# Performance work log

Hardware: AMD Instinct MI355X
Metric: run time of the kernel (lower is better)

The kernel has to match this reference:

```python
import jax, jax.numpy as jnp
import numpy as np

N = 20000
NNBR = 64
MESH = (64, 64, 64)
ORDER = 4          # B-spline interpolation order
ALPHA = 0.35       # Ewald splitting parameter (1/Angstrom)
BOX = 73.68        # cubic box edge (Angstrom)
KE = 14.399645478425668  # Coulomb constant, eV*Angstrom/e^2


def _Mn(x, n):
    """Cardinal B-spline M_n(x), support [0, n]."""
    if n == 2:
        return jnp.maximum(0.0, 1.0 - jnp.abs(x - 1.0))
    return (x * _Mn(x, n - 1) + (n - x) * _Mn(x - 1.0, n - 1)) / (n - 1)


def _bspline_fac(K):
    """|b(m)|^-2 ... i.e. 1/|Euler spline denominator|^2 per mesh dim."""
    m = jnp.arange(K, dtype=jnp.float32)
    k = jnp.arange(ORDER - 1, dtype=jnp.float32)
    Mv = _Mn(k + 1.0, ORDER)                       # M_n(1..n-1)
    phase = 2.0 * jnp.pi * m[:, None] * k[None, :] / K
    dre = jnp.sum(Mv * jnp.cos(phase), axis=1)
    dim = jnp.sum(Mv * jnp.sin(phase), axis=1)
    return 1.0 / (dre * dre + dim * dim)


def _pme_energy(positions, charges, cell, nbr, shifts):
    n = positions.shape[0]
    # ---------------- real-space short-range sum ----------------
    i_idx = jnp.arange(n)[:, None]
    valid = (nbr >= 0) & ~((nbr == i_idx) & jnp.all(shifts == 0, axis=-1))
    j = jnp.where(nbr >= 0, nbr, 0)
    rvec = positions[j] + shifts.astype(positions.dtype) @ cell - positions[:, None, :]
    r2 = jnp.sum(rvec * rvec, axis=-1)
    r = jnp.sqrt(jnp.where(valid, r2, 1.0))
    qq = charges[:, None] * charges[j]
    e_real = 0.5 * jnp.sum(jnp.where(valid, qq * jax.scipy.special.erfc(ALPHA * r) / r, 0.0))
    # ---------------- B-spline charge spreading ----------------
    Kx, Ky, Kz = MESH
    frac = positions @ jnp.linalg.inv(cell)        # cell rows = lattice vectors
    u = frac * jnp.array(MESH, dtype=positions.dtype)
    base = jnp.floor(u)
    t = u - base                                   # in [0, 1)
    basei = base.astype(jnp.int32)
    offs = jnp.arange(ORDER)
    wx = _Mn(t[:, 0:1] + offs, ORDER)              # [N, ORDER]
    wy = _Mn(t[:, 1:2] + offs, ORDER)
    wz = _Mn(t[:, 2:3] + offs, ORDER)
    ix = (basei[:, 0:1] - offs) % Kx
    iy = (basei[:, 1:2] - offs) % Ky
    iz = (basei[:, 2:3] - offs) % Kz
    W = (charges[:, None] * wx)[:, :, None, None] * wy[:, None, :, None] * wz[:, None, None, :]
    IDX = (ix[:, :, None, None] * Ky + iy[:, None, :, None]) * Kz + iz[:, None, None, :]
    mesh = jnp.zeros(Kx * Ky * Kz, positions.dtype).at[IDX.reshape(-1)].add(W.reshape(-1)).reshape(MESH)
    # ---------------- reciprocal-space FFT convolution ----------------
    Q = jnp.fft.fftn(mesh)
    Brec = 2.0 * jnp.pi * jnp.linalg.inv(cell).T   # rows are reciprocal vectors
    mx = (jnp.fft.fftfreq(Kx) * Kx).astype(positions.dtype)
    my = (jnp.fft.fftfreq(Ky) * Ky).astype(positions.dtype)
    mz = (jnp.fft.fftfreq(Kz) * Kz).astype(positions.dtype)
    kvec = (mx[:, None, None, None] * Brec[0] + my[None, :, None, None] * Brec[1]
            + mz[None, None, :, None] * Brec[2])
    k2 = jnp.sum(kvec * kvec, axis=-1)
    a2 = ALPHA * ALPHA
    kern = jnp.where(k2 > 0, jnp.exp(-k2 / (4.0 * a2)) / jnp.where(k2 > 0, k2, 1.0), 0.0)
    C = _bspline_fac(Kx)[:, None, None] * _bspline_fac(Ky)[None, :, None] * _bspline_fac(Kz)[None, None, :]
    vol = jnp.abs(jnp.linalg.det(cell))
    e_rec = (2.0 * jnp.pi / vol) * jnp.sum(kern * C * (Q.real ** 2 + Q.imag ** 2))
    # ---------------- self + neutralizing background ----------------
    qtot = jnp.sum(charges)
    e_self = -(ALPHA / jnp.sqrt(jnp.pi)) * jnp.sum(charges * charges)
    e_bg = -(jnp.pi / (2.0 * a2 * vol)) * qtot * qtot
    return e_real + e_rec + e_self + e_bg


def setup_inputs() -> dict:
    key = jax.random.key(0)
    k1, k2, k3 = jax.random.split(key, 3)
    positions = jax.random.uniform(k1, (N, 3), jnp.float32) * BOX
    q = jax.random.normal(k2, (N,), jnp.float32)
    q = q - jnp.mean(q)  # neutral system
    cell = BOX * jnp.eye(3, dtype=jnp.float32)
    nbr = jax.random.randint(k3, (N, NNBR), 0, N, jnp.int32)
    shifts = jnp.zeros((N, NNBR, 3), jnp.int32)
    return {"positions": positions, "node_charges": q, "cell": cell,
            "neighbor_matrix": nbr, "neighbor_shifts": shifts}


def reference(positions, node_charges, cell, neighbor_matrix, neighbor_shifts):
    def e_strain(pos, q, c, eps):
        F = jnp.eye(3, dtype=pos.dtype) + eps
        return _pme_energy(pos @ F, q, c @ F, neighbor_matrix, neighbor_shifts)

    eps0 = jnp.zeros((3, 3), positions.dtype)
    e, (g_pos, g_eps) = jax.value_and_grad(e_strain, argnums=(0, 3))(
        positions, node_charges, cell, eps0)
    vol = jnp.abs(jnp.linalg.det(cell))
    energies = e.reshape(1) * KE
    forces = -g_pos * KE
    virial = -0.5 * (g_eps + g_eps.T) * KE
    stresses = (virial / vol)[None]
    return energies, forces, stresses
```

## Files before the change

kernel.cpp:

```cpp
#include <hip/hip_runtime.h>
#include <math.h>

#define NATOM 20000
#define NNBR  64
#define KM    64
#define KM3   (KM*KM*KM)
#define NPAIR (NATOM*NNBR)

#define ALPHA_C 0.35f
#define KE_C    14.399645478425668f
#define TWO_OVER_SQRTPI 1.1283791670955126f
#define TWOPI_F 6.2831853071795864f
#define PI_F    3.14159265358979f
#define RC2     661.2244898f

#define WS_RE    0
#define WS_IM    (KM3)
#define WS_MESH  (2*KM3)
#define WS_GJ    (3*KM3)
#define WS_PART  (3*KM3 + 3*NATOM)
#define WS_FI    (WS_PART + 1024)
#define WS_POSQ  (WS_FI + 3*NATOM)
#define WS_NBS   (WS_POSQ + 4*NATOM)
#define ZERO_LEN (KM3 + 3*NATOM + 1024)

__device__ __forceinline__ float M2f(float x){ return fmaxf(0.f, 1.f - fabsf(x - 1.f)); }
__device__ __forceinline__ float M3f(float x){ return (x*M2f(x) + (3.f-x)*M2f(x-1.f)) * 0.5f; }
__device__ __forceinline__ float M4f(float x){ return (x*M3f(x) + (4.f-x)*M3f(x-1.f)) * (1.f/3.f); }

__device__ __forceinline__ float wsum64(float v){
#pragma unroll
  for(int off=32; off>0; off>>=1) v += __shfl_xor(v, off, 64);
  return v;
}

__device__ __forceinline__ float hinv9(const float* __restrict__ cell, float* h){
  float m00=cell[0],m01=cell[1],m02=cell[2];
  float m10=cell[3],m11=cell[4],m12=cell[5];
  float m20=cell[6],m21=cell[7],m22=cell[8];
  float det = m00*(m11*m22-m12*m21) - m01*(m10*m22-m12*m20) + m02*(m10*m21-m11*m20);
  float id = 1.f/det;
  h[0]=(m11*m22-m12*m21)*id; h[1]=(m02*m21-m01*m22)*id; h[2]=(m01*m12-m02*m11)*id;
  h[3]=(m12*m20-m10*m22)*id; h[4]=(m00*m22-m02*m20)*id; h[5]=(m02*m10-m00*m12)*id;
  h[6]=(m10*m21-m11*m20)*id; h[7]=(m01*m20-m00*m21)*id; h[8]=(m00*m11-m01*m10)*id;
  return fabsf(det);
}

__device__ __forceinline__ void fill_tw(int t, float* twr, float* twi){
  if(t < 64){
    float ss, cc; sincosf((TWOPI_F/64.f)*(float)t, &ss, &cc);
    twr[t] = cc; twi[t] = -ss;
  }
}

__device__ __forceinline__ void fft64t(float& xr, float& xi, int lane,
                                       const float* __restrict__ twr,
                                       const float* __restrict__ twi, float sgn){
#pragma unroll
  for(int k=0;k<6;k++){
    int half = 32 >> k;
    float or_ = __shfl_xor(xr, half, 64);
    float oi_ = __shfl_xor(xi, half, 64);
    bool hi = (lane & half) != 0;
    float sr = hi ? (or_ - xr) : (xr + or_);
    float si = hi ? (oi_ - xi) : (xi + oi_);
    int e = (lane & (half-1)) << k;
    float wr2 = hi ? twr[e] : 1.f;
    float wi2 = hi ? sgn*twi[e] : 0.f;
    xr = sr*wr2 - si*wi2;
    xi = sr*wi2 + si*wr2;
  }
  int rev = __brev((unsigned)lane) >> 26;
  xr = __shfl(xr, rev, 64);
  xi = __shfl(xi, rev, 64);
}

__global__ __launch_bounds__(256) void init_kernel(
    const float* __restrict__ pos, const float* __restrict__ q,
    const int* __restrict__ nbr, const int* __restrict__ shifts,
    float* __restrict__ zbase, float4* __restrict__ posq, int* __restrict__ nbs){
  int t = blockIdx.x*256 + threadIdx.x;
  if(t < ZERO_LEN) zbase[t] = 0.f;
  if(t < NATOM)
    posq[t] = make_float4(pos[3*t], pos[3*t+1], pos[3*t+2], q[t]);
  if(t < NPAIR){
    int j = nbr[t];
    int sx=shifts[3*t], sy=shifts[3*t+1], sz=shifts[3*t+2];
    int v;
    if(j < 0) v = -1;
    else v = (j & 0x7FFF) | ((sx+8)&15)<<15 | ((sy+8)&15)<<19 | ((sz+8)&15)<<23;
    nbs[t] = v;
  }
}

__global__ __launch_bounds__(256) void realspread_kernel(
    const float4* __restrict__ posq, const int* __restrict__ nbs,
    const float* __restrict__ cell,
    float* __restrict__ fi, float* __restrict__ gj, float* __restrict__ part,
    float* __restrict__ mesh){
  int lane = threadIdx.x & 63;
  if(blockIdx.x < 1250){
    int wid  = blockIdx.x*4 + (threadIdx.x>>6);
    int i0   = wid*4;
    float c0=cell[0],c1=cell[1],c2=cell[2];
    float c3=cell[3],c4=cell[4],c5=cell[5];
    float c6=cell[6],c7=cell[7],c8=cell[8];
    int v[4]; int jj[4]; float4 pi[4], pj[4];
#pragma unroll
    for(int k=0;k<4;k++) v[k]  = nbs[(i0+k)*NNBR + lane];
#pragma unroll
    for(int k=0;k<4;k++) pi[k] = posq[i0+k];
#pragma unroll
    for(int k=0;k<4;k++) jj[k] = min(v[k] & 0x7FFF, NATOM-1);
#pragma unroll
    for(int k=0;k<4;k++) pj[k] = posq[jj[k]];
    float e=0.f, vxx=0.f,vyy=0.f,vzz=0.f,vxy=0.f,vxz=0.f,vyz=0.f;
#pragma unroll
    for(int k=0;k<4;k++){
      int i = i0 + k;
      int vv = v[k], j = jj[k];
      int sx=((vv>>15)&15)-8, sy=((vv>>19)&15)-8, sz=((vv>>23)&15)-8;
      bool valid = (vv>=0) && !((j==i) && (sx==0) && (sy==0) && (sz==0));
      float rx = pj[k].x - pi[k].x + sx*c0 + sy*c3 + sz*c6;
      float ry = pj[k].y - pi[k].y + sx*c1 + sy*c4 + sz*c7;
      float rz = pj[k].z - pi[k].z + sx*c2 + sy*c5 + sz*c8;
      float r2 = rx*rx + ry*ry + rz*rz;
      float s = 0.f;
      if(valid && r2 > 0.f && r2 < RC2){
        float r = sqrtf(r2);
        float ar = ALPHA_C * r;
        float qq = pi[k].w * pj[k].w;
        float ef = erfcf(ar);
        float ex = expf(-ar*ar);
        float ir = 1.f/r;
        e += 0.5f*qq*ef*ir;
        s  = 0.5f*qq*(ef + TWO_OVER_SQRTPI*ar*ex)*ir*ir*ir;
      }
      float gx = s*rx, gy = s*ry, gz = s*rz;
      if(s != 0.f){
        unsafeAtomicAdd(&gj[3*j+0], -gx);
        unsafeAtomicAdd(&gj[3*j+1], -gy);
        unsafeAtomicAdd(&gj[3*j+2], -gz);
      }
      vxx -= s*rx*rx; vyy -= s*ry*ry; vzz -= s*rz*rz;
      vxy -= s*rx*ry; vxz -= s*rx*rz; vyz -= s*ry*rz;
      float tgx = wsum64(gx), tgy = wsum64(gy), tgz = wsum64(gz);
      if(lane==0){ fi[3*i]=tgx; fi[3*i+1]=tgy; fi[3*i+2]=tgz; }
    }
    e   = wsum64(e);
    vxx = wsum64(vxx); vyy = wsum64(vyy); vzz = wsum64(vzz);
    vxy = wsum64(vxy); vxz = wsum64(vxz); vyz = wsum64(vyz);
    if(lane==0){
      float* slot = part + (wid & 63)*16;
      unsafeAtomicAdd(&slot[0], e);
      unsafeAtomicAdd(&slot[1], vxx); unsafeAtomicAdd(&slot[2], vyy); unsafeAtomicAdd(&slot[3], vzz);
      unsafeAtomicAdd(&slot[4], vxy); unsafeAtomicAdd(&slot[5], vxz); unsafeAtomicAdd(&slot[6], vyz);
    }
  } else {
    int wid = (blockIdx.x - 1250)*4 + (threadIdx.x>>6);
    float h[9]; hinv9(cell, h);
    float4 pq = posq[wid];
    float u0=(pq.x*h[0]+pq.y*h[3]+pq.z*h[6])*(float)KM;
    float u1=(pq.x*h[1]+pq.y*h[4]+pq.z*h[7])*(float)KM;
    float u2=(pq.x*h[2]+pq.y*h[5]+pq.z*h[8])*(float)KM;
    float b0=floorf(u0), b1=floorf(u1), b2=floorf(u2);
    float t0=u0-b0, t1=u1-b1, t2=u2-b2;
    int i0=(int)b0, i1=(int)b1, i2=(int)b2;
    int a = lane>>4, b = (lane>>2)&3, c = lane&3;
    float w = pq.w * M4f(t0+(float)a) * M4f(t1+(float)b) * M4f(t2+(float)c);
    int ix=(i0-a+256)&63, iy=(i1-b+256)&63, iz=(i2-c+256)&63;
    unsafeAtomicAdd(&mesh[(ix*KM + iy)*KM + iz], w);
  }
}

__global__ __launch_bounds__(256) void fftZF(const float* __restrict__ mesh,
                                             float* __restrict__ re, float* __restrict__ im){
  __shared__ float twr[64], twi[64];
  int t = threadIdx.x, lane = t&63;
  fill_tw(t, twr, twi);
  __syncthreads();
  int idx = blockIdx.x*256 + t;
  float xr = mesh[idx], xi = 0.f;
  fft64t(xr, xi, lane, twr, twi, 1.f);
  re[idx]=xr; im[idx]=xi;
}

__global__ __launch_bounds__(256) void fftZI(float* __restrict__ re, const float* __restrict__ im){
  __shared__ float twr[64], twi[64];
  int t = threadIdx.x, lane = t&63;
  fill_tw(t, twr, twi);
  __syncthreads();
  int idx = blockIdx.x*256 + t;
  float xr = re[idx], xi = im[idx];
  fft64t(xr, xi, lane, twr, twi, -1.f);
  re[idx]=xr;
}

__global__ __launch_bounds__(256) void fftY(float* __restrict__ re, float* __restrict__ im,
                                            float sgn){
  __shared__ float lr[64][17], li[64][17], twr[64], twi[64];
  int t = threadIdx.x, lane = t&63, w = t>>6;
  fill_tw(t, twr, twi);
  int x = blockIdx.x>>2, z0 = (blockIdx.x&3)*16;
  int off = x*4096 + z0;
#pragma unroll
  for(int k=0;k<4;k++){
    int e = k*256 + t; int y = e>>4, zz = e&15;
    lr[y][zz] = re[off + y*64 + zz];
    li[y][zz] = im[off + y*64 + zz];
  }
  __syncthreads();
#pragma unroll
  for(int qq=0; qq<4; qq++){
    int zz = w*4 + qq;
    float xr = lr[lane][zz], xi = li[lane][zz];
    fft64t(xr, xi, lane, twr, twi, sgn);
    lr[lane][zz] = xr; li[lane][zz] = xi;
  }
  __syncthreads();
#pragma unroll
  for(int k=0;k<4;k++){
    int e = k*256 + t; int y = e>>4, zz = e&15;
    re[off + y*64 + zz] = lr[y][zz];
    im[off + y*64 + zz] = li[y][zz];
  }
}

__global__ __launch_bounds__(256) void fftBC(float* __restrict__ re, float* __restrict__ im,
                                             const float* __restrict__ cell,
                                             float* __restrict__ part){
  __shared__ float lr[64][17], li[64][17], cf[64], twr[64], twi[64];
  int t = threadIdx.x, lane = t&63, w = t>>6;
  int y = blockIdx.x>>2, z0 = (blockIdx.x&3)*16;
  float h[9]; hinv9(cell, h);
  fill_tw(t, twr, twi);
  if(t < 64){
    float p1 = TWOPI_F*(float)t/64.f;
    float s1,c1_,s2,c2_; sincosf(p1,&s1,&c1_); sincosf(2.f*p1,&s2,&c2_);
    float dre = (1.f/6.f) + (2.f/3.f)*c1_ + (1.f/6.f)*c2_;
    float dim = (2.f/3.f)*s1 + (1.f/6.f)*s2;
    cf[t] = 1.f/(dre*dre + dim*dim);
  }
  float* rp = re + y*64 + z0;
  float* ip = im + y*64 + z0;
#pragma unroll
  for(int k=0;k<4;k++){
    int e = k*256 + t; int xI = e>>4, zz = e&15;
    lr[xI][zz] = rp[xI*4096 + zz];
    li[xI][zz] = ip[xI*4096 + zz];
  }
  __syncthreads();
  const float inv4a2 = 1.f/(4.f*ALPHA_C*ALPHA_C);
  float my_f = (float)((y<32)? y : y-64);
  float sE=0.f, v0=0.f,v1=0.f,v2=0.f,v3=0.f,v4=0.f,v5=0.f;
#pragma unroll
  for(int qq=0; qq<4; qq++){
    int zz = w*4 + qq; int z = z0 + zz;
    float xr = lr[lane][zz], xi = li[lane][zz];
    fft64t(xr, xi, lane, twr, twi, 1.f);
    int mx = lane, mz = z;
    float fx = (float)((mx<32)? mx : mx-64);
    float fz = (float)((mz<32)? mz : mz-64);
    float kx = TWOPI_F*(fx*h[0] + my_f*h[1] + fz*h[2]);
    float ky = TWOPI_F*(fx*h[3] + my_f*h[4] + fz*h[5]);
    float kz = TWOPI_F*(fx*h[6] + my_f*h[7] + fz*h[8]);
    float k2 = kx*kx + ky*ky + kz*kz;
    float wk = 0.f;
    if(k2 > 0.f){
      float kern = expf(-k2*inv4a2)/k2;
      wk = kern * cf[mx]*cf[y]*cf[z];
      float q2 = xr*xr + xi*xi;
      sE += wk*q2;
      float fac = wk*q2*(inv4a2 + 1.f/k2)*2.f;
      v0 += fac*kx*kx; v1 += fac*ky*ky; v2 += fac*kz*kz;
      v3 += fac*kx*ky; v4 += fac*kx*kz; v5 += fac*ky*kz;
    }
    xr *= wk; xi *= wk;
    fft64t(xr, xi, lane, twr, twi, -1.f);
    lr[lane][zz] = xr; li[lane][zz] = xi;
  }
  __syncthreads();
#pragma unroll
  for(int k=0;k<4;k++){
    int e = k*256 + t; int xI = e>>4, zz = e&15;
    rp[xI*4096 + zz] = lr[xI][zz];
    ip[xI*4096 + zz] = li[xI][zz];
  }
  sE = wsum64(sE);
  v0 = wsum64(v0); v1 = wsum64(v1); v2 = wsum64(v2);
  v3 = wsum64(v3); v4 = wsum64(v4); v5 = wsum64(v5);
  if(lane==0){
    float* slot = part + (((blockIdx.x<<2)|w)&63)*16;
    unsafeAtomicAdd(&slot[7],  sE);
    unsafeAtomicAdd(&slot[8],  v0); unsafeAtomicAdd(&slot[9],  v1);
    unsafeAtomicAdd(&slot[10], v2); unsafeAtomicAdd(&slot[11], v3);
    unsafeAtomicAdd(&slot[12], v4); unsafeAtomicAdd(&slot[13], v5);
  }
}

__global__ __launch_bounds__(256) void gather_kernel(
    const float4* __restrict__ posq, const float* __restrict__ cell,
    const float* __restrict__ phi,
    const float* __restrict__ fi, const float* __restrict__ gj,
    const float* __restrict__ part, float* __restrict__ out){
  __shared__ float sa[256], sb[256], facc[16];
  int lane = threadIdx.x & 63;
  int wid  = blockIdx.x*4 + (threadIdx.x>>6);
  int i0   = wid*4;
  float h[9]; float V = hinv9(cell, h);
  int a = lane>>4, b = (lane>>2)&3, c = lane&3;
  float fa=(float)a, fb=(float)b, fc=(float)c;
  float4 pq[4];
#pragma unroll
  for(int k=0;k<4;k++) pq[k] = posq[i0+k];
  float t0[4], t1[4], t2[4]; float p[4];
#pragma unroll
  for(int k=0;k<4;k++){
    float u0=(pq[k].x*h[0]+pq[k].y*h[3]+pq[k].z*h[6])*(float)KM;
    float u1=(pq[k].x*h[1]+pq[k].y*h[4]+pq[k].z*h[7])*(float)KM;
    float u2=(pq[k].x*h[2]+pq[k].y*h[5]+pq[k].z*h[8])*(float)KM;
    float b0=floorf(u0), b1=floorf(u1), b2=floorf(u2);
    t0[k]=u0-b0; t1[k]=u1-b1; t2[k]=u2-b2;
    int ix=((int)b0-a+256)&63, iy=((int)b1-b+256)&63, iz=((int)b2-c+256)&63;
    p[k] = phi[(ix*KM + iy)*KM + iz];
  }
#pragma unroll
  for(int k=0;k<4;k++){
    float wxa=M4f(t0[k]+fa), wyb=M4f(t1[k]+fb), wzc=M4f(t2[k]+fc);
    float dxa=M3f(t0[k]+fa)-M3f(t0[k]+fa-1.f);
    float dyb=M3f(t1[k]+fb)-M3f(t1[k]+fb-1.f);
    float dzc=M3f(t2[k]+fc)-M3f(t2[k]+fc-1.f);
    float Sx = wsum64(p[k]*dxa*wyb*wzc);
    float Sy = wsum64(p[k]*wxa*dyb*wzc);
    float Sz = wsum64(p[k]*wxa*wyb*dzc);
    if(lane==0){
      int i = i0 + k;
      float scale = pq[k].w * (2.f*TWOPI_F/V) * (float)KM;
      float g0 = scale*(Sx*h[0] + Sy*h[1] + Sz*h[2]);
      float g1 = scale*(Sx*h[3] + Sy*h[4] + Sz*h[5]);
      float g2 = scale*(Sx*h[6] + Sy*h[7] + Sz*h[8]);
      out[1+3*i+0] = -KE_C*(fi[3*i+0] + gj[3*i+0] + g0);
      out[1+3*i+1] = -KE_C*(fi[3*i+1] + gj[3*i+1] + g1);
      out[1+3*i+2] = -KE_C*(fi[3*i+2] + gj[3*i+2] + g2);
    }
  }
  if(blockIdx.x==0){
    int t = threadIdx.x;
    float qa=0.f, qb=0.f;
    for(int i=t;i<NATOM;i+=256){ float qv=posq[i].w; qa+=qv; qb+=qv*qv; }
    sa[t]=qa; sb[t]=qb; __syncthreads();
    for(int off=128; off>0; off>>=1){
      if(t<off){ sa[t]+=sa[t+off]; sb[t]+=sb[t+off]; } __syncthreads();
    }
    if(t<14){ float s=0.f; for(int sl=0;sl<64;sl++) s+=part[sl*16+t]; facc[t]=s; }
    __syncthreads();
    if(t==0){
      float qtot = sa[0], sumq2 = sb[0];
      float a2 = ALPHA_C*ALPHA_C;
      float pref = TWOPI_F/V;
      float e_real = facc[0];
      float e_rec  = pref*facc[7];
      float e_self = -(ALPHA_C/sqrtf(PI_F))*sumq2;
      float e_bg   = -(PI_F/(2.f*a2*V))*qtot*qtot;
      out[0] = (e_real + e_rec + e_self + e_bg)*KE_C;
      float gxx = facc[1] + pref*facc[8]  - e_rec - e_bg;
      float gyy = facc[2] + pref*facc[9]  - e_rec - e_bg;
      float gzz = facc[3] + pref*facc[10] - e_rec - e_bg;
      float gxy = facc[4] + pref*facc[11];
      float gxz = facc[5] + pref*facc[12];
      float gyz = facc[6] + pref*facc[13];
      float cc = -KE_C/V;
      float* st = out + 1 + 3*NATOM;
      st[0]=cc*gxx; st[4]=cc*gyy; st[8]=cc*gzz;
      st[1]=cc*gxy; st[3]=cc*gxy;
      st[2]=cc*gxz; st[6]=cc*gxz;
      st[5]=cc*gyz; st[7]=cc*gyz;
    }
  }
}

extern "C" void kernel_launch(void* const* d_in, const int* in_sizes, int n_in,
                              void* d_out, int out_size, void* d_ws, size_t ws_size,
                              hipStream_t stream) {
  const float* pos  = (const float*)d_in[0];
  const float* q    = (const float*)d_in[1];
  const float* cell = (const float*)d_in[2];
  const int* nbr    = (const int*)d_in[3];
  const int* shifts = (const int*)d_in[4];
  float* out = (float*)d_out;
  float* ws  = (float*)d_ws;
  float*  bufRe = ws + WS_RE;
  float*  bufIm = ws + WS_IM;
  float*  mesh  = ws + WS_MESH;
  float*  gj    = ws + WS_GJ;
  float*  part  = ws + WS_PART;
  float*  fi    = ws + WS_FI;
  float4* posq  = (float4*)(ws + WS_POSQ);
  int*    nbs   = (int*)(ws + WS_NBS);

  init_kernel<<<(NPAIR+255)/256,256,0,stream>>>(pos, q, nbr, shifts, mesh, posq, nbs);
  realspread_kernel<<<6250,256,0,stream>>>(posq, nbs, cell, fi, gj, part, mesh);
  fftZF<<<1024,256,0,stream>>>(mesh, bufRe, bufIm);
  fftY <<< 256,256,0,stream>>>(bufRe, bufIm, 1.f);
  fftBC<<< 256,256,0,stream>>>(bufRe, bufIm, cell, part);
  fftY <<< 256,256,0,stream>>>(bufRe, bufIm, -1.f);
  fftZI<<<1024,256,0,stream>>>(bufRe, bufIm);
  gather_kernel<<<1250,256,0,stream>>>(posq, cell, bufRe, fi, gj, part, out);
}
```

Before: 179.8 us.

## Compact in-cutoff neighbor pairs into a list before the real-space sum

The init kernel now tests every neighbor pair against the cutoff and the validity rules. It appends the surviving pairs to a global list using a wave ballot plus one atomic counter per wave. The real-space kernel then runs a grid-stride loop over only the compacted pairs, so waves no longer sit idle on out-of-cutoff lanes during the erfc/exp work. In exchange, both i and j forces are now scattered with atomics (six per pair instead of three plus a wave reduction), the pair order becomes nondeterministic, and mesh zeroing switches to float4 stores.

Result: slower. 425.6 us (+136.7%).

```diff
diff --git a/kernel.cpp b/kernel.cpp
--- a/kernel.cpp
+++ b/kernel.cpp
@@ -17,12 +17,16 @@
 #define WS_RE    0
 #define WS_IM    (KM3)
 #define WS_MESH  (2*KM3)
-#define WS_GJ    (3*KM3)
+#define WS_GF    (3*KM3)
 #define WS_PART  (3*KM3 + 3*NATOM)
-#define WS_FI    (WS_PART + 1024)
-#define WS_POSQ  (WS_FI + 3*NATOM)
-#define WS_NBS   (WS_POSQ + 4*NATOM)
+#define WS_POSQ  (WS_PART + 1024)
+#define WS_PLIST (WS_POSQ + 4*NATOM)
+#define WS_CNT   (WS_PLIST + 2*NPAIR)
 #define ZERO_LEN (KM3 + 3*NATOM + 1024)
+#define ZB4      ((ZERO_LEN + 3)/4)
+#define FILT_BLOCKS 5000
+#define RBLOCKS  1250
+#define RSTRIDE  (RBLOCKS*256)
 
 __device__ __forceinline__ float M2f(float x){ return fmaxf(0.f, 1.f - fabsf(x - 1.f)); }
 __device__ __forceinline__ float M3f(float x){ return (x*M2f(x) + (3.f-x)*M2f(x-1.f)) * 0.5f; }
@@ -78,86 +82,92 @@
 __global__ __launch_bounds__(256) void init_kernel(
     const float* __restrict__ pos, const float* __restrict__ q,
     const int* __restrict__ nbr, const int* __restrict__ shifts,
-    float* __restrict__ zbase, float4* __restrict__ posq, int* __restrict__ nbs){
-  int t = blockIdx.x*256 + threadIdx.x;
-  if(t < ZERO_LEN) zbase[t] = 0.f;
-  if(t < NATOM)
-    posq[t] = make_float4(pos[3*t], pos[3*t+1], pos[3*t+2], q[t]);
-  if(t < NPAIR){
+    const float* __restrict__ cell,
+    float4* __restrict__ zmesh4, float4* __restrict__ posq,
+    int2* __restrict__ plist, int* __restrict__ cnt){
+  if(blockIdx.x < FILT_BLOCKS){
+    int lane = threadIdx.x & 63;
+    int i = blockIdx.x*4 + (threadIdx.x>>6);
+    int t = i*NNBR + lane;
     int j = nbr[t];
     int sx=shifts[3*t], sy=shifts[3*t+1], sz=shifts[3*t+2];
-    int v;
-    if(j < 0) v = -1;
-    else v = (j & 0x7FFF) | ((sx+8)&15)<<15 | ((sy+8)&15)<<19 | ((sz+8)&15)<<23;
-    nbs[t] = v;
-  }
-}
-
-__global__ __launch_bounds__(256) void realspread_kernel(
-    const float4* __restrict__ posq, const int* __restrict__ nbs,
-    const float* __restrict__ cell,
-    float* __restrict__ fi, float* __restrict__ gj, float* __restrict__ part,
-    float* __restrict__ mesh){
-  int lane = threadIdx.x & 63;
-  if(blockIdx.x < 1250){
-    int wid  = blockIdx.x*4 + (threadIdx.x>>6);
-    int i0   = wid*4;
+    int jc = j < 0 ? 0 : j;
     float c0=cell[0],c1=cell[1],c2=cell[2];
     float c3=cell[3],c4=cell[4],c5=cell[5];
     float c6=cell[6],c7=cell[7],c8=cell[8];
-    int v[4]; int jj[4]; float4 pi[4], pj[4];
-#pragma unroll
-    for(int k=0;k<4;k++) v[k]  = nbs[(i0+k)*NNBR + lane];
-#pragma unroll
-    for(int k=0;k<4;k++) pi[k] = posq[i0+k];
-#pragma unroll
-    for(int k=0;k<4;k++) jj[k] = min(v[k] & 0x7FFF, NATOM-1);
-#pragma unroll
-    for(int k=0;k<4;k++) pj[k] = posq[jj[k]];
+    float rx = pos[3*jc]   - pos[3*i]   + sx*c0 + sy*c3 + sz*c6;
+    float ry = pos[3*jc+1] - pos[3*i+1] + sx*c1 + sy*c4 + sz*c7;
+    float rz = pos[3*jc+2] - pos[3*i+2] + sx*c2 + sy*c5 + sz*c8;
+    float r2 = rx*rx + ry*ry + rz*rz;
+    bool valid = (j>=0) && !((j==i) && (sx==0) && (sy==0) && (sz==0))
+                 && (r2 > 0.f) && (r2 < RC2);
+    unsigned long long m = __ballot(valid);
+    int rank = __popcll(m & ((1ULL<<lane)-1ULL));
+    int tot  = __popcll(m);
+    int base = 0;
+    if(lane==0 && tot) base = atomicAdd(cnt, tot);
+    base = __shfl(base, 0, 64);
+    if(valid)
+      plist[base+rank] = make_int2(i | (j<<15),
+                                   (sx+8) | ((sy+8)<<4) | ((sz+8)<<8));
+  } else {
+    int t = (blockIdx.x - FILT_BLOCKS)*256 + threadIdx.x;
+    if(t < ZB4) zmesh4[t] = make_float4(0.f,0.f,0.f,0.f);
+    if(t < NATOM)
+      posq[t] = make_float4(pos[3*t], pos[3*t+1], pos[3*t+2], q[t]);
+  }
+}
+
+__global__ __launch_bounds__(256) void realspread_kernel(
+    const float4* __restrict__ posq, const int2* __restrict__ plist,
+    const int* __restrict__ cnt, const float* __restrict__ cell,
+    float* __restrict__ gf, float* __restrict__ part, float* __restrict__ mesh){
+  int lane = threadIdx.x & 63;
+  if(blockIdx.x < RBLOCKS){
+    int count = *cnt;
+    float c0=cell[0],c1=cell[1],c2=cell[2];
+    float c3=cell[3],c4=cell[4],c5=cell[5];
+    float c6=cell[6],c7=cell[7],c8=cell[8];
     float e=0.f, vxx=0.f,vyy=0.f,vzz=0.f,vxy=0.f,vxz=0.f,vyz=0.f;
-#pragma unroll
-    for(int k=0;k<4;k++){
-      int i = i0 + k;
-      int vv = v[k], j = jj[k];
-      int sx=((vv>>15)&15)-8, sy=((vv>>19)&15)-8, sz=((vv>>23)&15)-8;
-      bool valid = (vv>=0) && !((j==i) && (sx==0) && (sy==0) && (sz==0));
-      float rx = pj[k].x - pi[k].x + sx*c0 + sy*c3 + sz*c6;
-      float ry = pj[k].y - pi[k].y + sx*c1 + sy*c4 + sz*c7;
-      float rz = pj[k].z - pi[k].z + sx*c2 + sy*c5 + sz*c8;
+    for(int p = blockIdx.x*256 + threadIdx.x; p < count; p += RSTRIDE){
+      int2 pr = plist[p];
+      int i = pr.x & 0x7FFF, j = (pr.x>>15) & 0x7FFF;
+      int sx = (pr.y&15)-8, sy = ((pr.y>>4)&15)-8, sz = ((pr.y>>8)&15)-8;
+      float4 pi = posq[i];
+      float4 pj = posq[j];
+      float rx = pj.x - pi.x + sx*c0 + sy*c3 + sz*c6;
+      float ry = pj.y - pi.y + sx*c1 + sy*c4 + sz*c7;
+      float rz = pj.z - pi.z + sx*c2 + sy*c5 + sz*c8;
       float r2 = rx*rx + ry*ry + rz*rz;
-      float s = 0.f;
-      if(valid && r2 > 0.f && r2 < RC2){
-        float r = sqrtf(r2);
-        float ar = ALPHA_C * r;
-        float qq = pi[k].w * pj[k].w;
-        float ef = erfcf(ar);
-        float ex = expf(-ar*ar);
-        float ir = 1.f/r;
-        e += 0.5f*qq*ef*ir;
-        s  = 0.5f*qq*(ef + TWO_OVER_SQRTPI*ar*ex)*ir*ir*ir;
-      }
+      float r = sqrtf(r2);
+      float ar = ALPHA_C * r;
+      float qq = pi.w * pj.w;
+      float ef = erfcf(ar);
+      float ex = expf(-ar*ar);
+      float ir = 1.f/r;
+      e += 0.5f*qq*ef*ir;
+      float s = 0.5f*qq*(ef + TWO_OVER_SQRTPI*ar*ex)*ir*ir*ir;
       float gx = s*rx, gy = s*ry, gz = s*rz;
-      if(s != 0.f){
-        unsafeAtomicAdd(&gj[3*j+0], -gx);
-        unsafeAtomicAdd(&gj[3*j+1], -gy);
-        unsafeAtomicAdd(&gj[3*j+2], -gz);
-      }
+      unsafeAtomicAdd(&gf[3*i+0],  gx);
+      unsafeAtomicAdd(&gf[3*i+1],  gy);
+      unsafeAtomicAdd(&gf[3*i+2],  gz);
+      unsafeAtomicAdd(&gf[3*j+0], -gx);
+      unsafeAtomicAdd(&gf[3*j+1], -gy);
+      unsafeAtomicAdd(&gf[3*j+2], -gz);
       vxx -= s*rx*rx; vyy -= s*ry*ry; vzz -= s*rz*rz;
       vxy -= s*rx*ry; vxz -= s*rx*rz; vyz -= s*ry*rz;
-      float tgx = wsum64(gx), tgy = wsum64(gy), tgz = wsum64(gz);
-      if(lane==0){ fi[3*i]=tgx; fi[3*i+1]=tgy; fi[3*i+2]=tgz; }
     }
     e   = wsum64(e);
     vxx = wsum64(vxx); vyy = wsum64(vyy); vzz = wsum64(vzz);
     vxy = wsum64(vxy); vxz = wsum64(vxz); vyz = wsum64(vyz);
     if(lane==0){
-      float* slot = part + (wid & 63)*16;
+      float* slot = part + (((blockIdx.x<<2)|(threadIdx.x>>6)) & 63)*16;
       unsafeAtomicAdd(&slot[0], e);
       unsafeAtomicAdd(&slot[1], vxx); unsafeAtomicAdd(&slot[2], vyy); unsafeAtomicAdd(&slot[3], vzz);
       unsafeAtomicAdd(&slot[4], vxy); unsafeAtomicAdd(&slot[5], vxz); unsafeAtomicAdd(&slot[6], vyz);
     }
   } else {
-    int wid = (blockIdx.x - 1250)*4 + (threadIdx.x>>6);
+    int wid = (blockIdx.x - RBLOCKS)*4 + (threadIdx.x>>6);
     float h[9]; hinv9(cell, h);
     float4 pq = posq[wid];
     float u0=(pq.x*h[0]+pq.y*h[3]+pq.z*h[6])*(float)KM;
@@ -300,8 +310,7 @@
 
 __global__ __launch_bounds__(256) void gather_kernel(
     const float4* __restrict__ posq, const float* __restrict__ cell,
-    const float* __restrict__ phi,
-    const float* __restrict__ fi, const float* __restrict__ gj,
+    const float* __restrict__ phi, const float* __restrict__ gf,
     const float* __restrict__ part, float* __restrict__ out){
   __shared__ float sa[256], sb[256], facc[16];
   int lane = threadIdx.x & 63;
@@ -339,9 +348,9 @@
       float g0 = scale*(Sx*h[0] + Sy*h[1] + Sz*h[2]);
       float g1 = scale*(Sx*h[3] + Sy*h[4] + Sz*h[5]);
       float g2 = scale*(Sx*h[6] + Sy*h[7] + Sz*h[8]);
-      out[1+3*i+0] = -KE_C*(fi[3*i+0] + gj[3*i+0] + g0);
-      out[1+3*i+1] = -KE_C*(fi[3*i+1] + gj[3*i+1] + g1);
-      out[1+3*i+2] = -KE_C*(fi[3*i+2] + gj[3*i+2] + g2);
+      out[1+3*i+0] = -KE_C*(gf[3*i+0] + g0);
+      out[1+3*i+1] = -KE_C*(gf[3*i+1] + g1);
+      out[1+3*i+2] = -KE_C*(gf[3*i+2] + g2);
     }
   }
   if(blockIdx.x==0){
@@ -392,18 +401,20 @@
   float*  bufRe = ws + WS_RE;
   float*  bufIm = ws + WS_IM;
   float*  mesh  = ws + WS_MESH;
-  float*  gj    = ws + WS_GJ;
+  float*  gf    = ws + WS_GF;
   float*  part  = ws + WS_PART;
-  float*  fi    = ws + WS_FI;
   float4* posq  = (float4*)(ws + WS_POSQ);
-  int*    nbs   = (int*)(ws + WS_NBS);
-
-  init_kernel<<<(NPAIR+255)/256,256,0,stream>>>(pos, q, nbr, shifts, mesh, posq, nbs);
-  realspread_kernel<<<6250,256,0,stream>>>(posq, nbs, cell, fi, gj, part, mesh);
+  int2*   plist = (int2*)(ws + WS_PLIST);
+  int*    cnt   = (int*)(ws + WS_CNT);
+
+  hipMemsetAsync(cnt, 0, sizeof(int), stream);
+  init_kernel<<<FILT_BLOCKS + (ZB4+255)/256, 256, 0, stream>>>(
+      pos, q, nbr, shifts, cell, (float4*)mesh, posq, plist, cnt);
+  realspread_kernel<<<RBLOCKS+5000,256,0,stream>>>(posq, plist, cnt, cell, gf, part, mesh);
   fftZF<<<1024,256,0,stream>>>(mesh, bufRe, bufIm);
   fftY <<< 256,256,0,stream>>>(bufRe, bufIm, 1.f);
   fftBC<<< 256,256,0,stream>>>(bufRe, bufIm, cell, part);
   fftY <<< 256,256,0,stream>>>(bufRe, bufIm, -1.f);
   fftZI<<<1024,256,0,stream>>>(bufRe, bufIm);
-  gather_kernel<<<1250,256,0,stream>>>(posq, cell, bufRe, fi, gj, part, out);
-}
+  gather_kernel<<<1250,256,0,stream>>>(posq, cell, bufRe, gf, part, out);
+}
```
